# Optimization experiments

Hardware: AMD Instinct MI355X
Metric: run time of the kernel (lower is better)

Reference implementation:

```python
import jax, jax.numpy as jnp
from jax import lax
import numpy as np

S, ST, CI, K = 3, 2, 64, 7  # num_subset_S, num_subset_T, inter_channels, kernel_size


def _ln2(x, g, b, eps=1e-5):
    # LayerNorm over the last TWO dims (matches normalized_shape=[L, C])
    m = x.mean(axis=(-2, -1), keepdims=True)
    v = x.var(axis=(-2, -1), keepdims=True)
    return (x - m) / jnp.sqrt(v + eps) * g + b


def setup_inputs() -> dict:
    key = jax.random.key(0)
    ks = jax.random.split(key, 8)
    N, V, T, C = 32, 25, 64, 256
    g = lambda i, shape: jax.random.normal(ks[i], shape, jnp.float32) * 0.02
    return {
        "x": jax.random.normal(ks[0], (N, V, T, C), jnp.float32),
        "Wqk_s": g(1, (C, 2 * S * CI)), "bqk_s": jnp.zeros((2 * S * CI,), jnp.float32),
        "alphas": jnp.ones((1, 1, 1, S), jnp.float32),
        "attention0s": jnp.ones((1, V, V, S), jnp.float32) / V,
        "Wo_s": g(2, (S * C, C)), "bo_s": jnp.zeros((C,), jnp.float32),
        "g_os": jnp.ones((T, C), jnp.float32), "b_os": jnp.zeros((T, C), jnp.float32),
        "Wff_s": g(3, (C, C)), "bff_s": jnp.zeros((C,), jnp.float32),
        "g_ffs": jnp.ones((T, C), jnp.float32), "b_ffs": jnp.zeros((T, C), jnp.float32),
        "Wqk_t": g(4, (C, 4 * ST * CI)), "bqk_t": jnp.zeros((4 * ST * CI,), jnp.float32),
        "alphat_f": jnp.ones((1, 1, 1, ST), jnp.float32),
        "alphat_b": jnp.ones((1, 1, 1, ST), jnp.float32),
        "Wo_t": g(5, (2 * ST * C, C)), "bo_t": jnp.zeros((C,), jnp.float32),
        "g_ot": jnp.ones((V, C), jnp.float32), "b_ot": jnp.zeros((V, C), jnp.float32),
        "Wff_t": g(6, (C, C)), "bff_t": jnp.zeros((C,), jnp.float32),
        "g_fft": jnp.ones((V, C), jnp.float32), "b_fft": jnp.zeros((V, C), jnp.float32),
        "conv_w": g(7, (C, C, K, 1)), "conv_b": jnp.zeros((C,), jnp.float32),
        "bn_g": jnp.ones((C,), jnp.float32), "bn_b": jnp.zeros((C,), jnp.float32),
        "bn_m": jnp.zeros((C,), jnp.float32), "bn_v": jnp.ones((C,), jnp.float32),
    }


def reference(x, Wqk_s, bqk_s, alphas, attention0s, Wo_s, bo_s, g_os, b_os,
              Wff_s, bff_s, g_ffs, b_ffs, Wqk_t, bqk_t, alphat_f, alphat_b,
              Wo_t, bo_t, g_ot, b_ot, Wff_t, bff_t, g_fft, b_fft,
              conv_w, conv_b, bn_g, bn_b, bn_m, bn_v):
    N, V, T, C = x.shape
    gelu = lambda a: jax.nn.gelu(a, approximate=False)
    # ---- spatial multi-subset attention ----
    qk = (x @ Wqk_s + bqk_s).reshape(N, V, T, CI, 2 * S)
    q, k = qk[..., :S], qk[..., S:]
    att = jnp.tanh(jnp.einsum('nutcs,nvtcs->nuvs', q, k) / (CI * T)) * alphas + attention0s
    y = jnp.einsum('nutc,nuvs->nvtcs', x, att).reshape(N, V, T, S * C)
    y = gelu(x + _ln2(y @ Wo_s + bo_s, g_os, b_os))       # out_nets + residual (downs1=id)
    y = gelu(x + _ln2(y @ Wff_s + bff_s, g_ffs, b_ffs))   # ff_nets  + residual (downs2=id)
    y = y.transpose(0, 2, 1, 3)                            # (N,T,V,C)
    # ---- directed temporal attention ----
    qkt = (y @ Wqk_t + bqk_t).reshape(N, T, V, CI, 4 * ST)
    q_f, q_b = qkt[..., :ST], qkt[..., ST:2 * ST]
    k_f, k_b = qkt[..., 2 * ST:3 * ST], qkt[..., 3 * ST:]
    bmask = jnp.triu(jnp.ones((T, T), x.dtype))            # backward_mask; forward = transpose
    att_b = jnp.tanh(jnp.einsum('ntvcs,nqvcs->ntqs', q_b, k_b) / (CI * V)) * alphat_b * bmask[None, :, :, None]
    att_f = jnp.tanh(jnp.einsum('ntvcs,nqvcs->ntqs', q_f, k_f) / (CI * V)) * alphat_f * bmask.T[None, :, :, None]
    z_f = jnp.einsum('ntvc,ntqs->nqvcs', y, att_f).reshape(N, T, V, ST * C)
    z_b = jnp.einsum('ntvc,ntqs->nqvcs', y, att_b).reshape(N, T, V, ST * C)
    z = jnp.concatenate([z_f, z_b], axis=-1)               # (N,T,V,4C)
    z = gelu(y + _ln2(z @ Wo_t + bo_t, g_ot, b_ot))        # out_nett + residual (downt1=id)
    z = gelu(y + _ln2(z @ Wff_t + bff_t, g_fft, b_fft))    # ff_nett  + residual (downt2=id)
    # ---- TCN tail: (N,T,V,C) -> nctv ----
    zc = z.transpose(0, 3, 1, 2)                           # (N,C,T,V)
    pad = (K - 1) // 2
    z1 = lax.conv_general_dilated(zc, conv_w, (1, 1), [(pad, pad), (0, 0)],
                                  dimension_numbers=('NCHW', 'OIHW', 'NCHW'))
    z1 = z1 + conv_b[None, :, None, None]
    z1 = (z1 - bn_m[None, :, None, None]) / jnp.sqrt(bn_v + 1e-5)[None, :, None, None]
    z1 = z1 * bn_g[None, :, None, None] + bn_b[None, :, None, None]  # BatchNorm2d (eval)
    z1 = gelu(zc + z1)                                     # downt3 = identity
    return z1.transpose(0, 3, 2, 1)                        # nctv -> nvtc, (N,V,T,C)
```

## Files before the change

kernel.cpp:

```cpp
#include <hip/hip_runtime.h>

static constexpr int N_ = 32, V_ = 25, T_ = 64, C_ = 256;
static constexpr int S_ = 3, ST_ = 2, CI_ = 64, K_ = 7;
static constexpr int M_  = N_ * V_ * T_;
static constexpr int TC_ = T_ * C_;
static constexpr int VC_ = V_ * C_;
static constexpr long TOT_ = (long)M_ * C_;
static constexpr long PLANE_ = 2048L * 1600;

typedef __bf16 bf16x8 __attribute__((ext_vector_type(8)));
typedef float  f32x4  __attribute__((ext_vector_type(4)));

__device__ __forceinline__ float gelu_f(float x) {
    return 0.5f * x * (1.0f + erff(x * 0.70710678118654752f));
}
__device__ __forceinline__ ushort f2bf(float x) {
    uint u = __float_as_uint(x);
    u += 0x7fffu + ((u >> 16) & 1u);
    return (ushort)(u >> 16);
}
__device__ __forceinline__ float bf2f(ushort h) { return __uint_as_float((uint)h << 16); }

__device__ __forceinline__ int lofs(int row, int chunk) {
    return row * 32 + ((chunk ^ ((row >> 1) & 3)) << 3);
// ... 9 lines not shown
    hi[idx] = h;
    lo[idx] = f2bf(x - bf2f(h));
}
__global__ void prep_conv(const float* __restrict__ cw,
                          ushort* __restrict__ hi, ushort* __restrict__ lo) {
    int idx = blockIdx.x * 256 + threadIdx.x;
    if (idx >= K_ * C_ * C_) return;
    int kh = idx / (C_ * C_);
    int rem = idx % (C_ * C_);
    int o = rem >> 8, i = rem & 255;
    float x = cw[((long)o * C_ + i) * K_ + kh];
    ushort h = f2bf(x);
    hi[idx] = h;
    lo[idx] = f2bf(x - bf2f(h));
}

__global__ __launch_bounds__(256) void gemm_mfma(
    const float* __restrict__ A, int lda,
    const ushort* __restrict__ Wh, const ushort* __restrict__ Wl, int Kc,
    const float* __restrict__ bias,
    float* __restrict__ Out, int Nc)
{
    __shared__ ushort Ah[128 * 32], Al[128 * 32], Bh[128 * 32], Bl[128 * 32];
    const int tid = threadIdx.x;
    const int row0 = blockIdx.y * 128, col0 = blockIdx.x * 128;
    const int lane = tid & 63;
    const int wid = tid >> 6, wm = wid >> 1, wn = wid & 1;
    const int fr = lane & 15, fc = lane >> 4;
    const int r0 = tid >> 2, c0 = tid & 3;
    const int r1 = (tid + 256) >> 2, c1 = c0;
    const float*  arow0 = A + (long)(row0 + r0) * lda + c0 * 8;
    const float*  arow1 = A + (long)(row0 + r1) * lda + c1 * 8;
    const ushort* wrow0h = Wh + (long)(col0 + r0) * Kc + c0 * 8;
    const ushort* wrow0l = Wl + (long)(col0 + r0) * Kc + c0 * 8;
    const ushort* wrow1h = Wh + (long)(col0 + r1) * Kc + c1 * 8;
    const ushort* wrow1l = Wl + (long)(col0 + r1) * Kc + c1 * 8;
    const int la0 = lofs(r0, c0), la1 = lofs(r1, c1);

    float4 pa0, pa1, pa2, pa3;
    uint4 pw0h, pw0l, pw1h, pw1l;
    #define LOADK(k0) do { \
        pa0 = *(const float4*)(arow0 + (k0));      pa1 = *(const float4*)(arow0 + (k0) + 4); \
        pa2 = *(const float4*)(arow1 + (k0));      pa3 = *(const float4*)(arow1 + (k0) + 4); \
        pw0h = *(const uint4*)(wrow0h + (k0));     pw0l = *(const uint4*)(wrow0l + (k0)); \
        pw1h = *(const uint4*)(wrow1h + (k0));     pw1l = *(const uint4*)(wrow1l + (k0)); \
    } while (0)

    LOADK(0);
    f32x4 acc[4][4] = {};
    for (int k0 = 0; k0 < Kc; k0 += 32) {
        __syncthreads();
        {
            float f0[8] = {pa0.x, pa0.y, pa0.z, pa0.w, pa1.x, pa1.y, pa1.z, pa1.w};
            float f1[8] = {pa2.x, pa2.y, pa2.z, pa2.w, pa3.x, pa3.y, pa3.z, pa3.w};
            uint h0[4], l0[4], h1[4], l1[4];
            #pragma unroll
            for (int e = 0; e < 4; ++e) {
                ushort ha = f2bf(f0[2*e]), hb = f2bf(f0[2*e+1]);
                l0[e] = (uint)f2bf(f0[2*e] - bf2f(ha)) | ((uint)f2bf(f0[2*e+1] - bf2f(hb)) << 16);
                h0[e] = (uint)ha | ((uint)hb << 16);
                ushort hc = f2bf(f1[2*e]), hd = f2bf(f1[2*e+1]);
                l1[e] = (uint)f2bf(f1[2*e] - bf2f(hc)) | ((uint)f2bf(f1[2*e+1] - bf2f(hd)) << 16);
                h1[e] = (uint)hc | ((uint)hd << 16);
            }
            *(uint4*)&Ah[la0] = make_uint4(h0[0], h0[1], h0[2], h0[3]);
            *(uint4*)&Al[la0] = make_uint4(l0[0], l0[1], l0[2], l0[3]);
            *(uint4*)&Ah[la1] = make_uint4(h1[0], h1[1], h1[2], h1[3]);
            *(uint4*)&Al[la1] = make_uint4(l1[0], l1[1], l1[2], l1[3]);
            *(uint4*)&Bh[la0] = pw0h;  *(uint4*)&Bl[la0] = pw0l;
            *(uint4*)&Bh[la1] = pw1h;  *(uint4*)&Bl[la1] = pw1l;
        }
        __syncthreads();
        if (k0 + 32 < Kc) LOADK(k0 + 32);
        bf16x8 fah[4], fal[4];
        #pragma unroll
        for (int i = 0; i < 4; ++i) {
            int rA = wm * 64 + i * 16 + fr;
            int oA = lofs(rA, fc);
            fah[i] = *(bf16x8*)&Ah[oA];
            fal[i] = *(bf16x8*)&Al[oA];
        }
        #pragma unroll
        for (int j = 0; j < 4; ++j) {
            int rW = wn * 64 + j * 16 + fr;
            int oW = lofs(rW, fc);
            bf16x8 wh = *(bf16x8*)&Bh[oW];
            bf16x8 wl = *(bf16x8*)&Bl[oW];
            #pragma unroll
            for (int i = 0; i < 4; ++i) {
                acc[i][j] = __builtin_amdgcn_mfma_f32_16x16x32_bf16(fah[i], wh, acc[i][j], 0, 0, 0);
                acc[i][j] = __builtin_amdgcn_mfma_f32_16x16x32_bf16(fah[i], wl, acc[i][j], 0, 0, 0);
                acc[i][j] = __builtin_amdgcn_mfma_f32_16x16x32_bf16(fal[i], wh, acc[i][j], 0, 0, 0);
            }
        }
    }
    #undef LOADK
    float bv[4]; int colv[4];
    #pragma unroll
    for (int j = 0; j < 4; ++j) {
        colv[j] = col0 + wn * 64 + j * 16 + fr;
        bv[j] = bias ? bias[colv[j]] : 0.0f;
    }
    #pragma unroll
    for (int i = 0; i < 4; ++i) {
        long rbase = row0 + wm * 64 + i * 16 + fc * 4;
        #pragma unroll
        for (int r = 0; r < 4; ++r) {
            long ob = (rbase + r) * (long)Nc;
            #pragma unroll
            for (int j = 0; j < 4; ++j)
                Out[ob + colv[j]] = acc[i][j][r] + bv[j];
        }
    }
}

__global__ __launch_bounds__(256) void conv_bn_gelu(
    const float* __restrict__ Z,
    const ushort* __restrict__ Wh, const ushort* __restrict__ Wl,
    const float* __restrict__ conv_b, const float* __restrict__ bn_g,
    const float* __restrict__ bn_b,  const float* __restrict__ bn_m,
    const float* __restrict__ bn_v,
    float* __restrict__ Out)
{
    __shared__ ushort Ah[128 * 32], Al[128 * 32], Bh[128 * 32], Bl[128 * 32];
    const int tid = threadIdx.x;
    const int row0 = blockIdx.y * 128, col0 = blockIdx.x * 128;
    const int lane = tid & 63;
    const int wid = tid >> 6, wm = wid >> 1, wn = wid & 1;
    const int fr = lane & 15, fc = lane >> 4;
    const int r0 = tid >> 2, c0 = tid & 3;
    const int r1 = (tid + 256) >> 2, c1 = c0;
    const int la0 = lofs(r0, c0), la1 = lofs(r1, c1);
    const int m0 = row0 + r0, m1 = row0 + r1;
    const int t0g = (m0 / V_) % T_, t1g = (m1 / V_) % T_;

    float4 pa0, pa1, pa2, pa3;
    uint4 pw0h, pw0l, pw1h, pw1l;
    auto loadk = [&](int kt) {
        const int kh = kt >> 3, kc = (kt & 7) * 32, d = kh - 3;
        const float z4[4] = {0, 0, 0, 0};
        if (t0g + d >= 0 && t0g + d < T_) {
            const float* zr = Z + (long)(m0 + d * V_) * C_ + kc + c0 * 8;
            pa0 = *(const float4*)zr; pa1 = *(const float4*)(zr + 4);
        } else { pa0 = *(const float4*)z4; pa1 = *(const float4*)z4; }
        if (t1g + d >= 0 && t1g + d < T_) {
            const float* zr = Z + (long)(m1 + d * V_) * C_ + kc + c1 * 8;
            pa2 = *(const float4*)zr; pa3 = *(const float4*)(zr + 4);
        } else { pa2 = *(const float4*)z4; pa3 = *(const float4*)z4; }
        const ushort* w0 = Wh + (long)kh * C_ * C_ + (long)(col0 + r0) * C_ + kc + c0 * 8;
        const ushort* w1 = Wh + (long)kh * C_ * C_ + (long)(col0 + r1) * C_ + kc + c1 * 8;
        const ushort* v0 = Wl + (long)kh * C_ * C_ + (long)(col0 + r0) * C_ + kc + c0 * 8;
        const ushort* v1 = Wl + (long)kh * C_ * C_ + (long)(col0 + r1) * C_ + kc + c1 * 8;
        pw0h = *(const uint4*)w0; pw0l = *(const uint4*)v0;
        pw1h = *(const uint4*)w1; pw1l = *(const uint4*)v1;
    };

    loadk(0);
    f32x4 acc[4][4] = {};
    for (int kt = 0; kt < K_ * 8; ++kt) {
        __syncthreads();
        {
            float f0[8] = {pa0.x, pa0.y, pa0.z, pa0.w, pa1.x, pa1.y, pa1.z, pa1.w};
            float f1[8] = {pa2.x, pa2.y, pa2.z, pa2.w, pa3.x, pa3.y, pa3.z, pa3.w};
            uint h0[4], l0[4], h1[4], l1[4];
            #pragma unroll
            for (int e = 0; e < 4; ++e) {
                ushort ha = f2bf(f0[2*e]), hb = f2bf(f0[2*e+1]);
                l0[e] = (uint)f2bf(f0[2*e] - bf2f(ha)) | ((uint)f2bf(f0[2*e+1] - bf2f(hb)) << 16);
                h0[e] = (uint)ha | ((uint)hb << 16);
                ushort hc = f2bf(f1[2*e]), hd = f2bf(f1[2*e+1]);
                l1[e] = (uint)f2bf(f1[2*e] - bf2f(hc)) | ((uint)f2bf(f1[2*e+1] - bf2f(hd)) << 16);
                h1[e] = (uint)hc | ((uint)hd << 16);
            }
            *(uint4*)&Ah[la0] = make_uint4(h0[0], h0[1], h0[2], h0[3]);
            *(uint4*)&Al[la0] = make_uint4(l0[0], l0[1], l0[2], l0[3]);
            *(uint4*)&Ah[la1] = make_uint4(h1[0], h1[1], h1[2], h1[3]);
            *(uint4*)&Al[la1] = make_uint4(l1[0], l1[1], l1[2], l1[3]);
            *(uint4*)&Bh[la0] = pw0h;  *(uint4*)&Bl[la0] = pw0l;
            *(uint4*)&Bh[la1] = pw1h;  *(uint4*)&Bl[la1] = pw1l;
        }
        __syncthreads();
        if (kt + 1 < K_ * 8) loadk(kt + 1);
        bf16x8 fah[4], fal[4];
        #pragma unroll
        for (int i = 0; i < 4; ++i) {
            int rA = wm * 64 + i * 16 + fr;
            int oA = lofs(rA, fc);
            fah[i] = *(bf16x8*)&Ah[oA];
            fal[i] = *(bf16x8*)&Al[oA];
        }
        #pragma unroll
        for (int j = 0; j < 4; ++j) {
            int rW = wn * 64 + j * 16 + fr;
            int oW = lofs(rW, fc);
            bf16x8 wh = *(bf16x8*)&Bh[oW];
            bf16x8 wl = *(bf16x8*)&Bl[oW];
            #pragma unroll
            for (int i = 0; i < 4; ++i) {
                acc[i][j] = __builtin_amdgcn_mfma_f32_16x16x32_bf16(fah[i], wh, acc[i][j], 0, 0, 0);
                acc[i][j] = __builtin_amdgcn_mfma_f32_16x16x32_bf16(fah[i], wl, acc[i][j], 0, 0, 0);
                acc[i][j] = __builtin_amdgcn_mfma_f32_16x16x32_bf16(fal[i], wh, acc[i][j], 0, 0, 0);
            }
        }
    }
    float cbv[4], scv[4], shv[4]; int colv[4];
    #pragma unroll
    for (int j = 0; j < 4; ++j) {
        int c = col0 + wn * 64 + j * 16 + fr;
        colv[j] = c;
// ... 4 lines not shown
    }
    #pragma unroll
    for (int i = 0; i < 4; ++i)
        #pragma unroll
        for (int r = 0; r < 4; ++r) {
            int m = row0 + wm * 64 + i * 16 + fc * 4 + r;
            int n = m / (T_ * V_);
            int rem = m % (T_ * V_);
            int t = rem / V_, v = rem % V_;
            long ob = (((long)n * V_ + v) * T_ + t) * C_;
            long zb = (long)m * C_;
            #pragma unroll
            for (int j = 0; j < 4; ++j) {
                float cv = acc[i][j][r] + cbv[j];
                float bn = cv * scv[j] + shv[j];
                Out[ob + colv[j]] = gelu_f(Z[zb + colv[j]] + bn);
            }
        }
}

__global__ void zero_f32(float* __restrict__ p, int n) {
    int i = blockIdx.x * 256 + threadIdx.x;
    if (i < n) p[i] = 0.0f;
}

__global__ __launch_bounds__(256) void att_s_partial(
    const float* __restrict__ QK,
    float* __restrict__ attPre)
{
    const int n = blockIdx.x;
    const int tg = blockIdx.y;
// ... 50 lines not shown
        a[s][uv] = attS[((long)n * V_ * V_ + uv) * S_ + s];
    }
    __syncthreads();
    float acc[V_] = {};
    for (int u = 0; u < V_; ++u) {
        const float* g = G + ((long)((n * V_ + u) * T_) + t) * 768 + c;
        float v0 = g[0], v1 = g[256], v2 = g[512];
        const float* a0 = &a[0][u * V_], *a1 = &a[1][u * V_], *a2 = &a[2][u * V_];
        #pragma unroll
        for (int v = 0; v < V_; ++v)
            acc[v] += a0[v] * v0 + a1[v] * v1 + a2[v] * v2;
    }
    const float b = bias[c];
    for (int v = 0; v < V_; ++v)
        P[((long)(n * V_ + v) * T_ + t) * C_ + c] = acc[v] + b;
}

__global__ void qkt_repack(const float* __restrict__ QKT,
                           ushort* __restrict__ QPh, ushort* __restrict__ QPl) {
    long idx = (long)blockIdx.x * 256 + threadIdx.x;
    if (idx >= (long)M_ * CI_) return;
    int m = (int)(idx >> 6), ci = (int)(idx & 63);
    int n = m / (T_ * V_);
    int rem = m % (T_ * V_);
    int t = rem / V_, v = rem % V_;
    const float* src = QKT + (long)m * 512 + ci * 8;
    float4 s0 = *(const float4*)src;
    float4 s1 = *(const float4*)(src + 4);
    float f[8] = {s0.x, s0.y, s0.z, s0.w, s1.x, s1.y, s1.z, s1.w};
    long rowk = ((long)(n * T_ + t)) * 1600 + v * 64 + ci;
    #pragma unroll
    for (int chan = 0; chan < 8; ++chan) {
        ushort h = f2bf(f[chan]);
        QPh[(long)chan * PLANE_ + rowk] = h;
        QPl[(long)chan * PLANE_ + rowk] = f2bf(f[chan] - bf2f(h));
    }
}

__global__ __launch_bounds__(256) void att_t_mfma(
    const ushort* __restrict__ QPh, const ushort* __restrict__ QPl,
    float* __restrict__ part)
{
    const int ks = blockIdx.x, pair = blockIdx.y, n = blockIdx.z;
    const int kbeg = (ks * 50) / 4, kend = ((ks + 1) * 50) / 4;
    __shared__ ushort Qh[64 * 32], Ql[64 * 32], Kh[64 * 32], Kl[64 * 32];
    const int tid = threadIdx.x;
    const int lane = tid & 63;
    const int wid = tid >> 6, wm = wid >> 1, wn = wid & 1;
    const int fr = lane & 15, fc = lane >> 4;
    const int tr = tid >> 2, tc = tid & 3;
    const long rowoff = ((long)n * T_ + tr) * 1600 + tc * 8;
// ... 11 lines not shown
    f32x4 acc[2][2] = {};
    for (int kstep = kbeg; kstep < kend; ++kstep) {
        __syncthreads();
        *(uint4*)&Qh[la] = pqh;  *(uint4*)&Ql[la] = pql;
        *(uint4*)&Kh[la] = pkh;  *(uint4*)&Kl[la] = pkl;
        __syncthreads();
        if (kstep + 1 < kend) {
            pqh = *(const uint4*)(qh_g + (kstep + 1) * 32);
            pql = *(const uint4*)(ql_g + (kstep + 1) * 32);
            pkh = *(const uint4*)(kh_g + (kstep + 1) * 32);
            pkl = *(const uint4*)(kl_g + (kstep + 1) * 32);
        }
        bf16x8 ah[2], al[2];
        #pragma unroll
        for (int i = 0; i < 2; ++i) {
            int rA = wm * 32 + i * 16 + fr;
            int oA = lofs(rA, fc);
            ah[i] = *(bf16x8*)&Qh[oA];
            al[i] = *(bf16x8*)&Ql[oA];
        }
        #pragma unroll
        for (int j = 0; j < 2; ++j) {
            int rB = wn * 32 + j * 16 + fr;
            int oB = lofs(rB, fc);
            bf16x8 bh = *(bf16x8*)&Kh[oB];
            bf16x8 bl = *(bf16x8*)&Kl[oB];
            #pragma unroll
            for (int i = 0; i < 2; ++i) {
                acc[i][j] = __builtin_amdgcn_mfma_f32_16x16x32_bf16(ah[i], bh, acc[i][j], 0, 0, 0);
                acc[i][j] = __builtin_amdgcn_mfma_f32_16x16x32_bf16(ah[i], bl, acc[i][j], 0, 0, 0);
                acc[i][j] = __builtin_amdgcn_mfma_f32_16x16x32_bf16(al[i], bh, acc[i][j], 0, 0, 0);
            }
        }
    }
    float* pb = part + (((long)ks * N_ + n) * 4 + pair) * 4096;
    #pragma unroll
    for (int i = 0; i < 2; ++i)
        #pragma unroll
        for (int r = 0; r < 4; ++r) {
// ... 50 lines not shown
        const float* g = G + ((long)((n * T_ + t) * V_) + v) * 512 + c;
        float v0 = g[0], v1 = g[256];
        const float* ar0 = &a[t * T_ + ty * 16];
        const float* ar1 = ar0 + T_ * T_;
        #pragma unroll
        for (int i = 0; i < 16; ++i) acc[i] += ar0[i] * v0 + ar1[i] * v1;
    }
    for (int i = 0; i < 16; ++i) {
        int q = ty * 16 + i;
        long idx = ((long)n * T_ + q) * VC_ + col;
        if (INIT) P[idx] = acc[i] + bias[c];
        else      P[idx] += acc[i];
    }
}

template <bool TR>
__global__ __launch_bounds__(256) void ln_res_gelu_TC(
    const float* __restrict__ P, const float* __restrict__ X,
    const float* __restrict__ G, const float* __restrict__ B,
    float* __restrict__ Out)
{
    const int g = blockIdx.x;
    const int n = g / V_, v = g % V_;
    const float* p = P + (long)g * TC_;
    const float* x = X + (long)g * TC_;
    float s = 0.f, ss = 0.f;
    for (int i = threadIdx.x; i < TC_; i += 256) { float a = p[i]; s += a; ss += a * a; }
    __shared__ float rs[4], rss[4];
    #pragma unroll
    for (int off = 32; off > 0; off >>= 1) { s += __shfl_down(s, off); ss += __shfl_down(ss, off); }
    if ((threadIdx.x & 63) == 0) { rs[threadIdx.x >> 6] = s; rss[threadIdx.x >> 6] = ss; }
    __syncthreads();
    s = rs[0] + rs[1] + rs[2] + rs[3];
    ss = rss[0] + rss[1] + rss[2] + rss[3];
    const float mean = s * (1.0f / TC_);
    const float var  = ss * (1.0f / TC_) - mean * mean;
    const float rstd = rsqrtf(var + 1e-5f);
    for (int i = threadIdx.x; i < TC_; i += 256) {
        float val = (p[i] - mean) * rstd * G[i] + B[i];
        float r = gelu_f(x[i] + val);
        if (TR) {
            int t = i >> 8, c = i & 255;
            Out[(((long)n * T_ + t) * V_ + v) * C_ + c] = r;
        } else {
            Out[(long)g * TC_ + i] = r;
        }
    }
}

__global__ __launch_bounds__(256) void ln_res_gelu_VC(
    const float* __restrict__ P, const float* __restrict__ X,
    const float* __restrict__ G, const float* __restrict__ B,
    float* __restrict__ Out)
{
    const int g = blockIdx.x;
    const float* p = P + (long)g * VC_;
    const float* x = X + (long)g * VC_;
    float s = 0.f, ss = 0.f;
    for (int i = threadIdx.x; i < VC_; i += 256) { float a = p[i]; s += a; ss += a * a; }
    __shared__ float rs[4], rss[4];
    #pragma unroll
    for (int off = 32; off > 0; off >>= 1) { s += __shfl_down(s, off); ss += __shfl_down(ss, off); }
    if ((threadIdx.x & 63) == 0) { rs[threadIdx.x >> 6] = s; rss[threadIdx.x >> 6] = ss; }
    __syncthreads();
    s = rs[0] + rs[1] + rs[2] + rs[3];
    ss = rss[0] + rss[1] + rss[2] + rss[3];
    const float mean = s * (1.0f / VC_);
    const float var  = ss * (1.0f / VC_) - mean * mean;
    const float rstd = rsqrtf(var + 1e-5f);
    for (int i = threadIdx.x; i < VC_; i += 256) {
        float val = (p[i] - mean) * rstd * G[i] + B[i];
        Out[(long)g * VC_ + i] = gelu_f(x[i] + val);
    }
}

extern "C" void kernel_launch(void* const* d_in, const int* in_sizes, int n_in,
                              void* d_out, int out_size, void* d_ws, size_t ws_size,
                              hipStream_t stream)
{
    const float* x        = (const float*)d_in[0];
    const float* Wqk_s    = (const float*)d_in[1];
    const float* bqk_s    = (const float*)d_in[2];
    const float* alphas   = (const float*)d_in[3];
    const float* att0s    = (const float*)d_in[4];
    const float* Wo_s     = (const float*)d_in[5];
    const float* bo_s     = (const float*)d_in[6];
    const float* g_os     = (const float*)d_in[7];
// ... 9 lines not shown
    const float* Wo_t     = (const float*)d_in[17];
    const float* bo_t     = (const float*)d_in[18];
    const float* g_ot     = (const float*)d_in[19];
    const float* b_ot     = (const float*)d_in[20];
    const float* Wff_t    = (const float*)d_in[21];
    const float* bff_t    = (const float*)d_in[22];
    const float* g_fft    = (const float*)d_in[23];
    const float* b_fft    = (const float*)d_in[24];
    const float* conv_w   = (const float*)d_in[25];
    const float* conv_b   = (const float*)d_in[26];
    const float* bn_g     = (const float*)d_in[27];
    const float* bn_b     = (const float*)d_in[28];
    const float* bn_m     = (const float*)d_in[29];
    const float* bn_v     = (const float*)d_in[30];

    float* B  = (float*)d_ws;
    float* B0  = B;
    float* B13 = B + TOT_;
    float* B26 = B + 2 * TOT_;
    float* B39 = B + 3 * TOT_;
    float* RA  = B + 4 * TOT_;
    float* attPre = RA;
    float* attS   = attPre + N_*V_*V_*S_;
    float* attF   = attS   + N_*V_*V_*S_;
    float* attB   = attF   + (long)N_*2*T_*T_;
    float* part   = attB   + (long)N_*2*T_*T_;
    ushort* wp = (ushort*)(part + 4L*N_*4*4096);
    ushort* qs_h = wp;  wp += 384*256;   ushort* qs_l = wp;  wp += 384*256;
    ushort* os_h = wp;  wp += 768*256;   ushort* os_l = wp;  wp += 768*256;
    ushort* fs_h = wp;  wp += 256*256;   ushort* fs_l = wp;  wp += 256*256;
    ushort* qt_h = wp;  wp += 512*256;   ushort* qt_l = wp;  wp += 512*256;
    ushort* ot0_h= wp;  wp += 512*256;   ushort* ot0_l= wp;  wp += 512*256;
    ushort* ot1_h= wp;  wp += 512*256;   ushort* ot1_l= wp;  wp += 512*256;
    ushort* ft_h = wp;  wp += 256*256;   ushort* ft_l = wp;  wp += 256*256;
    ushort* cv_h = wp;  wp += K_*256*256; ushort* cv_l = wp;
    ushort* QPh = (ushort*)B26;
    ushort* QPl = QPh + 8 * PLANE_;
    float* YT = (float*)d_out;

    auto prepw = [&](const float* W, int Kc, int Nc, ushort* h, ushort* l) {
        prep_w<<<(Kc*Nc + 255)/256, 256, 0, stream>>>(W, Kc, Nc, h, l);
    };
    prepw(Wqk_s, C_, 384, qs_h, qs_l);
    prepw(Wo_s,  C_, 768, os_h, os_l);
    prepw(Wff_s, C_, 256, fs_h, fs_l);
    prepw(Wqk_t, C_, 512, qt_h, qt_l);
    prepw(Wo_t,                      C_, 512, ot0_h, ot0_l);
    prepw(Wo_t + (long)ST_*C_*C_,    C_, 512, ot1_h, ot1_l);
    prepw(Wff_t, C_, 256, ft_h, ft_l);
    prep_conv<<<(K_*C_*C_ + 255)/256, 256, 0, stream>>>(conv_w, cv_h, cv_l);

    gemm_mfma<<<dim3(384/128, M_/128), 256, 0, stream>>>(x, C_, qs_h, qs_l, C_, bqk_s, B0, 384);
    zero_f32<<<(N_*V_*V_*S_ + 255)/256, 256, 0, stream>>>(attPre, N_*V_*V_*S_);
    att_s_partial<<<dim3(N_, 8), 256, 0, stream>>>(B0, attPre);
    att_s_final<<<(N_*V_*V_*S_ + 255)/256, 256, 0, stream>>>(attPre, alphas, att0s, attS);
    gemm_mfma<<<dim3(768/128, M_/128), 256, 0, stream>>>(x, C_, os_h, os_l, C_, nullptr, B0, 768);
    vmix_all<<<dim3(T_, N_), 256, 0, stream>>>(B0, attS, bo_s, B39);
    ln_res_gelu_TC<false><<<N_*V_, 256, 0, stream>>>(B39, x, g_os, b_os, B0);
    gemm_mfma<<<dim3(256/128, M_/128), 256, 0, stream>>>(B0, C_, fs_h, fs_l, C_, bff_s, B13, 256);
    ln_res_gelu_TC<true><<<N_*V_, 256, 0, stream>>>(B13, x, g_ffs, b_ffs, YT);

    gemm_mfma<<<dim3(512/128, M_/128), 256, 0, stream>>>(YT, C_, qt_h, qt_l, C_, bqk_t, B0, 512);
    qkt_repack<<<(int)(((long)M_*CI_ + 255)/256), 256, 0, stream>>>(B0, QPh, QPl);
    att_t_mfma<<<dim3(4, 4, N_), 256, 0, stream>>>(QPh, QPl, part);
    att_t_final<<<(N_*4*4096 + 255)/256, 256, 0, stream>>>(part, alphat_f, alphat_b, attF, attB);
    gemm_mfma<<<dim3(512/128, M_/128), 256, 0, stream>>>(YT, C_, ot0_h, ot0_l, C_, nullptr, B26, 512);
    tmix_all<true><<<dim3(VC_/64, N_), 256, 0, stream>>>(B26, attF, bo_t, B0);
    gemm_mfma<<<dim3(512/128, M_/128), 256, 0, stream>>>(YT, C_, ot1_h, ot1_l, C_, nullptr, B26, 512);
    tmix_all<false><<<dim3(VC_/64, N_), 256, 0, stream>>>(B26, attB, nullptr, B0);
    ln_res_gelu_VC<<<N_*T_, 256, 0, stream>>>(B0, YT, g_ot, b_ot, B13);
    gemm_mfma<<<dim3(256/128, M_/128), 256, 0, stream>>>(B13, C_, ft_h, ft_l, C_, bff_t, B26, 256);
    ln_res_gelu_VC<<<N_*T_, 256, 0, stream>>>(B26, YT, g_fft, b_fft, B39);

    conv_bn_gelu<<<dim3(C_/128, M_/128), 256, 0, stream>>>(B39, cv_h, cv_l, conv_b, bn_g, bn_b, bn_m, bn_v, (float*)d_out);
}
```

Before: 1.480 ms.

## Pre-split activations into bf16 hi/lo planes in producer kernels, feeding GEMMs directly

```diff
diff --git a/kernel.cpp b/kernel.cpp
--- a/kernel.cpp
+++ b/kernel.cpp
@@ -7,6 +7,7 @@
 static constexpr int VC_ = V_ * C_;
 static constexpr long TOT_ = (long)M_ * C_;
 static constexpr long PLANE_ = 2048L * 1600;
+static constexpr int TP_ = T_ + 6;
 
 typedef __bf16 bf16x8 __attribute__((ext_vector_type(8)));
 typedef float  f32x4  __attribute__((ext_vector_type(4)));
@@ -47,12 +48,33 @@
     hi[idx] = h;
     lo[idx] = f2bf(x - bf2f(h));
 }
-
-__global__ __launch_bounds__(256) void gemm_mfma(
-    const float* __restrict__ A, int lda,
-    const ushort* __restrict__ Wh, const ushort* __restrict__ Wl, int Kc,
+__global__ void prep_x(const float* __restrict__ X,
+                       ushort* __restrict__ Xh, ushort* __restrict__ Xl) {
+    long i = (long)blockIdx.x * 256 + threadIdx.x;
+    if (i >= TOT_) return;
+    float v = X[i];
+    ushort h = f2bf(v);
+    Xh[i] = h;
+    Xl[i] = f2bf(v - bf2f(h));
+}
+__global__ void zero_pad(ushort* __restrict__ Zph, ushort* __restrict__ Zpl) {
+    int idx = blockIdx.x * 256 + threadIdx.x;
+    if (idx >= N_ * 6 * V_ * C_) return;
+    int n = idx / (6 * V_ * C_);
+    int rem = idx % (6 * V_ * C_);
+    int tpi = rem / (V_ * C_), vc = rem % (V_ * C_);
+    int tp = (tpi < 3) ? tpi : (64 + tpi);
+    long o = ((long)(n * TP_ + tp) * V_) * C_ + vc;
+    Zph[o] = 0; Zpl[o] = 0;
+}
+
+template <bool PLANES>
+__global__ __launch_bounds__(256) void gemm_bf(
+    const ushort* __restrict__ Agh, const ushort* __restrict__ Agl,
+    const ushort* __restrict__ Wh,  const ushort* __restrict__ Wl,
     const float* __restrict__ bias,
-    float* __restrict__ Out, int Nc)
+    float* __restrict__ Out, int Nc,
+    ushort* __restrict__ Ph, ushort* __restrict__ Pl)
 {
     __shared__ ushort Ah[128 * 32], Al[128 * 32], Bh[128 * 32], Bl[128 * 32];
     const int tid = threadIdx.x;
@@ -61,62 +83,39 @@
     const int wid = tid >> 6, wm = wid >> 1, wn = wid & 1;
     const int fr = lane & 15, fc = lane >> 4;
     const int r0 = tid >> 2, c0 = tid & 3;
-    const int r1 = (tid + 256) >> 2, c1 = c0;
-    const float*  arow0 = A + (long)(row0 + r0) * lda + c0 * 8;
-    const float*  arow1 = A + (long)(row0 + r1) * lda + c1 * 8;
-    const ushort* wrow0h = Wh + (long)(col0 + r0) * Kc + c0 * 8;
-    const ushort* wrow0l = Wl + (long)(col0 + r0) * Kc + c0 * 8;
-    const ushort* wrow1h = Wh + (long)(col0 + r1) * Kc + c1 * 8;
-    const ushort* wrow1l = Wl + (long)(col0 + r1) * Kc + c1 * 8;
-    const int la0 = lofs(r0, c0), la1 = lofs(r1, c1);
-
-    float4 pa0, pa1, pa2, pa3;
-    uint4 pw0h, pw0l, pw1h, pw1l;
-    #define LOADK(k0) do { \
-        pa0 = *(const float4*)(arow0 + (k0));      pa1 = *(const float4*)(arow0 + (k0) + 4); \
-        pa2 = *(const float4*)(arow1 + (k0));      pa3 = *(const float4*)(arow1 + (k0) + 4); \
-        pw0h = *(const uint4*)(wrow0h + (k0));     pw0l = *(const uint4*)(wrow0l + (k0)); \
-        pw1h = *(const uint4*)(wrow1h + (k0));     pw1l = *(const uint4*)(wrow1l + (k0)); \
-    } while (0)
-
-    LOADK(0);
+    const long a0off = (long)(row0 + r0) * 256 + c0 * 8;
+    const long a1off = (long)(row0 + r0 + 64) * 256 + c0 * 8;
+    const long w0off = (long)(col0 + r0) * 256 + c0 * 8;
+    const long w1off = (long)(col0 + r0 + 64) * 256 + c0 * 8;
+    const int la0 = lofs(r0, c0), la1 = lofs(r0 + 64, c0);
+
+    uint4 p0, p1, p2, p3, p4, p5, p6, p7;
+    #define LD(k0) do { \
+        p0 = *(const uint4*)(Agh + a0off + (k0)); p1 = *(const uint4*)(Agh + a1off + (k0)); \
+        p2 = *(const uint4*)(Agl + a0off + (k0)); p3 = *(const uint4*)(Agl + a1off + (k0)); \
+        p4 = *(const uint4*)(Wh  + w0off + (k0)); p5 = *(const uint4*)(Wh  + w1off + (k0)); \
+        p6 = *(const uint4*)(Wl  + w0off + (k0)); p7 = *(const uint4*)(Wl  + w1off + (k0)); } while (0)
+
+    LD(0);
     f32x4 acc[4][4] = {};
-    for (int k0 = 0; k0 < Kc; k0 += 32) {
-        __syncthreads();
-        {
-            float f0[8] = {pa0.x, pa0.y, pa0.z, pa0.w, pa1.x, pa1.y, pa1.z, pa1.w};
-            float f1[8] = {pa2.x, pa2.y, pa2.z, pa2.w, pa3.x, pa3.y, pa3.z, pa3.w};
-            uint h0[4], l0[4], h1[4], l1[4];
-            #pragma unroll
-            for (int e = 0; e < 4; ++e) {
-                ushort ha = f2bf(f0[2*e]), hb = f2bf(f0[2*e+1]);
-                l0[e] = (uint)f2bf(f0[2*e] - bf2f(ha)) | ((uint)f2bf(f0[2*e+1] - bf2f(hb)) << 16);
-                h0[e] = (uint)ha | ((uint)hb << 16);
-                ushort hc = f2bf(f1[2*e]), hd = f2bf(f1[2*e+1]);
-                l1[e] = (uint)f2bf(f1[2*e] - bf2f(hc)) | ((uint)f2bf(f1[2*e+1] - bf2f(hd)) << 16);
-                h1[e] = (uint)hc | ((uint)hd << 16);
-            }
-            *(uint4*)&Ah[la0] = make_uint4(h0[0], h0[1], h0[2], h0[3]);
-            *(uint4*)&Al[la0] = make_uint4(l0[0], l0[1], l0[2], l0[3]);
-            *(uint4*)&Ah[la1] = make_uint4(h1[0], h1[1], h1[2], h1[3]);
-            *(uint4*)&Al[la1] = make_uint4(l1[0], l1[1], l1[2], l1[3]);
-            *(uint4*)&Bh[la0] = pw0h;  *(uint4*)&Bl[la0] = pw0l;
-            *(uint4*)&Bh[la1] = pw1h;  *(uint4*)&Bl[la1] = pw1l;
-        }
-        __syncthreads();
-        if (k0 + 32 < Kc) LOADK(k0 + 32);
+    for (int k0 = 0; k0 < 256; k0 += 32) {
+        __syncthreads();
+        *(uint4*)&Ah[la0] = p0;  *(uint4*)&Ah[la1] = p1;
+        *(uint4*)&Al[la0] = p2;  *(uint4*)&Al[la1] = p3;
+        *(uint4*)&Bh[la0] = p4;  *(uint4*)&Bh[la1] = p5;
+        *(uint4*)&Bl[la0] = p6;  *(uint4*)&Bl[la1] = p7;
+        __syncthreads();
+        if (k0 + 32 < 256) LD(k0 + 32);
         bf16x8 fah[4], fal[4];
         #pragma unroll
         for (int i = 0; i < 4; ++i) {
-            int rA = wm * 64 + i * 16 + fr;
-            int oA = lofs(rA, fc);
+            int oA = lofs(wm * 64 + i * 16 + fr, fc);
             fah[i] = *(bf16x8*)&Ah[oA];
             fal[i] = *(bf16x8*)&Al[oA];
         }
         #pragma unroll
         for (int j = 0; j < 4; ++j) {
-            int rW = wn * 64 + j * 16 + fr;
-            int oW = lofs(rW, fc);
+            int oW = lofs(wn * 64 + j * 16 + fr, fc);
             bf16x8 wh = *(bf16x8*)&Bh[oW];
             bf16x8 wl = *(bf16x8*)&Bl[oW];
             #pragma unroll
@@ -127,28 +126,52 @@
             }
         }
     }
-    #undef LOADK
+    #undef LD
     float bv[4]; int colv[4];
     #pragma unroll
     for (int j = 0; j < 4; ++j) {
         colv[j] = col0 + wn * 64 + j * 16 + fr;
         bv[j] = bias ? bias[colv[j]] : 0.0f;
     }
-    #pragma unroll
-    for (int i = 0; i < 4; ++i) {
-        long rbase = row0 + wm * 64 + i * 16 + fc * 4;
-        #pragma unroll
-        for (int r = 0; r < 4; ++r) {
-            long ob = (rbase + r) * (long)Nc;
+    if (!PLANES) {
+        #pragma unroll
+        for (int i = 0; i < 4; ++i) {
+            long rbase = row0 + wm * 64 + i * 16 + fc * 4;
             #pragma unroll
-            for (int j = 0; j < 4; ++j)
-                Out[ob + colv[j]] = acc[i][j][r] + bv[j];
+            for (int r = 0; r < 4; ++r) {
+                long ob = (rbase + r) * (long)Nc;
+                #pragma unroll
+                for (int j = 0; j < 4; ++j)
+                    Out[ob + colv[j]] = acc[i][j][r] + bv[j];
+            }
+        }
+    } else {
+        #pragma unroll
+        for (int i = 0; i < 4; ++i) {
+            #pragma unroll
+            for (int r = 0; r < 4; ++r) {
+                int m = row0 + wm * 64 + i * 16 + fc * 4 + r;
+                int n = m / (T_ * V_);
+                int rem = m % (T_ * V_);
+                int t = rem / V_, v = rem % V_;
+                long rk = ((long)(n * T_ + t)) * 1600 + v * 64;
+                #pragma unroll
+                for (int j = 0; j < 4; ++j) {
+                    int col = colv[j];
+                    int chan = col & 7, ci = col >> 3;
+                    float val = acc[i][j][r] + bv[j];
+                    ushort h = f2bf(val);
+                    Ph[(long)chan * PLANE_ + rk + ci] = h;
+                    Pl[(long)chan * PLANE_ + rk + ci] = f2bf(val - bf2f(h));
+                }
+            }
         }
     }
 }
 
 __global__ __launch_bounds__(256) void conv_bn_gelu(
-    const float* __restrict__ Z,
+    const ushort* __restrict__ Zph, const ushort* __restrict__ Zpl,
+    const float* __restrict__ Zres,
     const ushort* __restrict__ Wh, const ushort* __restrict__ Wl,
     const float* __restrict__ conv_b, const float* __restrict__ bn_g,
     const float* __restrict__ bn_b,  const float* __restrict__ bn_m,
@@ -162,70 +185,51 @@
     const int wid = tid >> 6, wm = wid >> 1, wn = wid & 1;
     const int fr = lane & 15, fc = lane >> 4;
     const int r0 = tid >> 2, c0 = tid & 3;
-    const int r1 = (tid + 256) >> 2, c1 = c0;
-    const int la0 = lofs(r0, c0), la1 = lofs(r1, c1);
-    const int m0 = row0 + r0, m1 = row0 + r1;
-    const int t0g = (m0 / V_) % T_, t1g = (m1 / V_) % T_;
-
-    float4 pa0, pa1, pa2, pa3;
-    uint4 pw0h, pw0l, pw1h, pw1l;
+    const int la0 = lofs(r0, c0), la1 = lofs(r0 + 64, c0);
+    const int m0 = row0 + r0, m1 = row0 + r0 + 64;
+    const int n0 = m0 / (T_ * V_), q0 = m0 % (T_ * V_);
+    const int n1 = m1 / (T_ * V_), q1 = m1 % (T_ * V_);
+    const long a0base = ((long)(n0 * TP_ + q0 / V_) * V_ + q0 % V_) * 256 + c0 * 8;
+    const long a1base = ((long)(n1 * TP_ + q1 / V_) * V_ + q1 % V_) * 256 + c0 * 8;
+    const long w0base = (long)(col0 + r0) * 256 + c0 * 8;
+    const long w1base = (long)(col0 + r0 + 64) * 256 + c0 * 8;
+
+    uint4 p0, p1, p2, p3, p4, p5, p6, p7;
     auto loadk = [&](int kt) {
-        const int kh = kt >> 3, kc = (kt & 7) * 32, d = kh - 3;
-        const float z4[4] = {0, 0, 0, 0};
-        if (t0g + d >= 0 && t0g + d < T_) {
-            const float* zr = Z + (long)(m0 + d * V_) * C_ + kc + c0 * 8;
-            pa0 = *(const float4*)zr; pa1 = *(const float4*)(zr + 4);
-        } else { pa0 = *(const float4*)z4; pa1 = *(const float4*)z4; }
-        if (t1g + d >= 0 && t1g + d < T_) {
-            const float* zr = Z + (long)(m1 + d * V_) * C_ + kc + c1 * 8;
-            pa2 = *(const float4*)zr; pa3 = *(const float4*)(zr + 4);
-        } else { pa2 = *(const float4*)z4; pa3 = *(const float4*)z4; }
-        const ushort* w0 = Wh + (long)kh * C_ * C_ + (long)(col0 + r0) * C_ + kc + c0 * 8;
-        const ushort* w1 = Wh + (long)kh * C_ * C_ + (long)(col0 + r1) * C_ + kc + c1 * 8;
-        const ushort* v0 = Wl + (long)kh * C_ * C_ + (long)(col0 + r0) * C_ + kc + c0 * 8;
-        const ushort* v1 = Wl + (long)kh * C_ * C_ + (long)(col0 + r1) * C_ + kc + c1 * 8;
-        pw0h = *(const uint4*)w0; pw0l = *(const uint4*)v0;
-        pw1h = *(const uint4*)w1; pw1l = *(const uint4*)v1;
+        const int kh = kt >> 3;
+        const long kc = (kt & 7) * 32;
+        const long ao = (long)kh * V_ * 256;
+        p0 = *(const uint4*)(Zph + a0base + ao + kc);
+        p1 = *(const uint4*)(Zph + a1base + ao + kc);
+        p2 = *(const uint4*)(Zpl + a0base + ao + kc);
+        p3 = *(const uint4*)(Zpl + a1base + ao + kc);
+        const long wo = (long)kh * 65536 + kc;
+        p4 = *(const uint4*)(Wh + w0base + wo);
+        p5 = *(const uint4*)(Wh + w1base + wo);
+        p6 = *(const uint4*)(Wl + w0base + wo);
+        p7 = *(const uint4*)(Wl + w1base + wo);
     };
 
     loadk(0);
     f32x4 acc[4][4] = {};
     for (int kt = 0; kt < K_ * 8; ++kt) {
         __syncthreads();
-        {
-            float f0[8] = {pa0.x, pa0.y, pa0.z, pa0.w, pa1.x, pa1.y, pa1.z, pa1.w};
-            float f1[8] = {pa2.x, pa2.y, pa2.z, pa2.w, pa3.x, pa3.y, pa3.z, pa3.w};
-            uint h0[4], l0[4], h1[4], l1[4];
-            #pragma unroll
-            for (int e = 0; e < 4; ++e) {
-                ushort ha = f2bf(f0[2*e]), hb = f2bf(f0[2*e+1]);
-                l0[e] = (uint)f2bf(f0[2*e] - bf2f(ha)) | ((uint)f2bf(f0[2*e+1] - bf2f(hb)) << 16);
-                h0[e] = (uint)ha | ((uint)hb << 16);
-                ushort hc = f2bf(f1[2*e]), hd = f2bf(f1[2*e+1]);
-                l1[e] = (uint)f2bf(f1[2*e] - bf2f(hc)) | ((uint)f2bf(f1[2*e+1] - bf2f(hd)) << 16);
-                h1[e] = (uint)hc | ((uint)hd << 16);
-            }
-            *(uint4*)&Ah[la0] = make_uint4(h0[0], h0[1], h0[2], h0[3]);
-            *(uint4*)&Al[la0] = make_uint4(l0[0], l0[1], l0[2], l0[3]);
-            *(uint4*)&Ah[la1] = make_uint4(h1[0], h1[1], h1[2], h1[3]);
-            *(uint4*)&Al[la1] = make_uint4(l1[0], l1[1], l1[2], l1[3]);
-            *(uint4*)&Bh[la0] = pw0h;  *(uint4*)&Bl[la0] = pw0l;
-            *(uint4*)&Bh[la1] = pw1h;  *(uint4*)&Bl[la1] = pw1l;
-        }
+        *(uint4*)&Ah[la0] = p0;  *(uint4*)&Ah[la1] = p1;
+        *(uint4*)&Al[la0] = p2;  *(uint4*)&Al[la1] = p3;
+        *(uint4*)&Bh[la0] = p4;  *(uint4*)&Bh[la1] = p5;
+        *(uint4*)&Bl[la0] = p6;  *(uint4*)&Bl[la1] = p7;
         __syncthreads();
         if (kt + 1 < K_ * 8) loadk(kt + 1);
         bf16x8 fah[4], fal[4];
         #pragma unroll
         for (int i = 0; i < 4; ++i) {
-            int rA = wm * 64 + i * 16 + fr;
-            int oA = lofs(rA, fc);
+            int oA = lofs(wm * 64 + i * 16 + fr, fc);
             fah[i] = *(bf16x8*)&Ah[oA];
             fal[i] = *(bf16x8*)&Al[oA];
         }
         #pragma unroll
         for (int j = 0; j < 4; ++j) {
-            int rW = wn * 64 + j * 16 + fr;
-            int oW = lofs(rW, fc);
+            int oW = lofs(wn * 64 + j * 16 + fr, fc);
             bf16x8 wh = *(bf16x8*)&Bh[oW];
             bf16x8 wl = *(bf16x8*)&Bl[oW];
             #pragma unroll
@@ -260,7 +264,7 @@
             for (int j = 0; j < 4; ++j) {
                 float cv = acc[i][j][r] + cbv[j];
                 float bn = cv * scv[j] + shv[j];
-                Out[ob + colv[j]] = gelu_f(Z[zb + colv[j]] + bn);
+                Out[ob + colv[j]] = gelu_f(Zres[zb + colv[j]] + bn);
             }
         }
 }
@@ -341,27 +345,6 @@
     const float b = bias[c];
     for (int v = 0; v < V_; ++v)
         P[((long)(n * V_ + v) * T_ + t) * C_ + c] = acc[v] + b;
-}
-
-__global__ void qkt_repack(const float* __restrict__ QKT,
-                           ushort* __restrict__ QPh, ushort* __restrict__ QPl) {
-    long idx = (long)blockIdx.x * 256 + threadIdx.x;
-    if (idx >= (long)M_ * CI_) return;
-    int m = (int)(idx >> 6), ci = (int)(idx & 63);
-    int n = m / (T_ * V_);
-    int rem = m % (T_ * V_);
-    int t = rem / V_, v = rem % V_;
-    const float* src = QKT + (long)m * 512 + ci * 8;
-    float4 s0 = *(const float4*)src;
-    float4 s1 = *(const float4*)(src + 4);
-    float f[8] = {s0.x, s0.y, s0.z, s0.w, s1.x, s1.y, s1.z, s1.w};
-    long rowk = ((long)(n * T_ + t)) * 1600 + v * 64 + ci;
-    #pragma unroll
-    for (int chan = 0; chan < 8; ++chan) {
-        ushort h = f2bf(f[chan]);
-        QPh[(long)chan * PLANE_ + rowk] = h;
-        QPl[(long)chan * PLANE_ + rowk] = f2bf(f[chan] - bf2f(h));
-    }
 }
 
 __global__ __launch_bounds__(256) void att_t_mfma(
@@ -403,15 +386,13 @@
         bf16x8 ah[2], al[2];
         #pragma unroll
         for (int i = 0; i < 2; ++i) {
-            int rA = wm * 32 + i * 16 + fr;
-            int oA = lofs(rA, fc);
+            int oA = lofs(wm * 32 + i * 16 + fr, fc);
             ah[i] = *(bf16x8*)&Qh[oA];
             al[i] = *(bf16x8*)&Ql[oA];
         }
         #pragma unroll
         for (int j = 0; j < 2; ++j) {
-            int rB = wn * 32 + j * 16 + fr;
-            int oB = lofs(rB, fc);
+            int oB = lofs(wn * 32 + j * 16 + fr, fc);
             bf16x8 bh = *(bf16x8*)&Kh[oB];
             bf16x8 bl = *(bf16x8*)&Kl[oB];
             #pragma unroll
@@ -492,63 +473,96 @@
     }
 }
 
-template <bool TR>
-__global__ __launch_bounds__(256) void ln_res_gelu_TC(
+#define LN_STATS(PBASE, L)                                                     \
+    float s = 0.f, ss = 0.f;                                                   \
+    for (int i = threadIdx.x; i < L; i += 256) { float a = (PBASE)[i]; s += a; ss += a * a; } \
+    __shared__ float rs[4], rss[4];                                            \
+    _Pragma("unroll")                                                          \
+    for (int off = 32; off > 0; off >>= 1) { s += __shfl_down(s, off); ss += __shfl_down(ss, off); } \
+    if ((threadIdx.x & 63) == 0) { rs[threadIdx.x >> 6] = s; rss[threadIdx.x >> 6] = ss; } \
+    __syncthreads();                                                           \
+    s = rs[0] + rs[1] + rs[2] + rs[3];                                         \
+    ss = rss[0] + rss[1] + rss[2] + rss[3];                                    \
+    const float mean = s * (1.0f / (L));                                       \
+    const float var  = ss * (1.0f / (L)) - mean * mean;                        \
+    const float rstd = rsqrtf(var + 1e-5f);
+
+__global__ __launch_bounds__(256) void ln_tc_y(
     const float* __restrict__ P, const float* __restrict__ X,
     const float* __restrict__ G, const float* __restrict__ B,
-    float* __restrict__ Out)
+    ushort* __restrict__ Oh, ushort* __restrict__ Ol)
+{
+    const int g = blockIdx.x;
+    const float* p = P + (long)g * TC_;
+    const float* x = X + (long)g * TC_;
+    LN_STATS(p, TC_)
+    for (int i = threadIdx.x; i < TC_; i += 256) {
+        float val = (p[i] - mean) * rstd * G[i] + B[i];
+        float r = gelu_f(x[i] + val);
+        ushort h = f2bf(r);
+        Oh[(long)g * TC_ + i] = h;
+        Ol[(long)g * TC_ + i] = f2bf(r - bf2f(h));
+    }
+}
+
+__global__ __launch_bounds__(256) void ln_tc_yt(
+    const float* __restrict__ P, const float* __restrict__ X,
+    const float* __restrict__ G, const float* __restrict__ B,
+    float* __restrict__ OutF, ushort* __restrict__ Oh, ushort* __restrict__ Ol)
 {
     const int g = blockIdx.x;
     const int n = g / V_, v = g % V_;
     const float* p = P + (long)g * TC_;
     const float* x = X + (long)g * TC_;
-    float s = 0.f, ss = 0.f;
-    for (int i = threadIdx.x; i < TC_; i += 256) { float a = p[i]; s += a; ss += a * a; }
-    __shared__ float rs[4], rss[4];
-    #pragma unroll
-    for (int off = 32; off > 0; off >>= 1) { s += __shfl_down(s, off); ss += __shfl_down(ss, off); }
-    if ((threadIdx.x & 63) == 0) { rs[threadIdx.x >> 6] = s; rss[threadIdx.x >> 6] = ss; }
-    __syncthreads();
-    s = rs[0] + rs[1] + rs[2] + rs[3];
-    ss = rss[0] + rss[1] + rss[2] + rss[3];
-    const float mean = s * (1.0f / TC_);
-    const float var  = ss * (1.0f / TC_) - mean * mean;
-    const float rstd = rsqrtf(var + 1e-5f);
+    LN_STATS(p, TC_)
     for (int i = threadIdx.x; i < TC_; i += 256) {
         float val = (p[i] - mean) * rstd * G[i] + B[i];
         float r = gelu_f(x[i] + val);
-        if (TR) {
-            int t = i >> 8, c = i & 255;
-            Out[(((long)n * T_ + t) * V_ + v) * C_ + c] = r;
-        } else {
-            Out[(long)g * TC_ + i] = r;
-        }
-    }
-}
-
-__global__ __launch_bounds__(256) void ln_res_gelu_VC(
+        int t = i >> 8, c = i & 255;
+        long o = (((long)n * T_ + t) * V_ + v) * C_ + c;
+        OutF[o] = r;
+        ushort h = f2bf(r);
+        Oh[o] = h;
+        Ol[o] = f2bf(r - bf2f(h));
+    }
+}
+
+__global__ __launch_bounds__(256) void ln_vc_z(
     const float* __restrict__ P, const float* __restrict__ X,
     const float* __restrict__ G, const float* __restrict__ B,
-    float* __restrict__ Out)
+    ushort* __restrict__ Oh, ushort* __restrict__ Ol)
 {
     const int g = blockIdx.x;
     const float* p = P + (long)g * VC_;
     const float* x = X + (long)g * VC_;
-    float s = 0.f, ss = 0.f;
-    for (int i = threadIdx.x; i < VC_; i += 256) { float a = p[i]; s += a; ss += a * a; }
-    __shared__ float rs[4], rss[4];
-    #pragma unroll
-    for (int off = 32; off > 0; off >>= 1) { s += __shfl_down(s, off); ss += __shfl_down(ss, off); }
-    if ((threadIdx.x & 63) == 0) { rs[threadIdx.x >> 6] = s; rss[threadIdx.x >> 6] = ss; }
-    __syncthreads();
-    s = rs[0] + rs[1] + rs[2] + rs[3];
-    ss = rss[0] + rss[1] + rss[2] + rss[3];
-    const float mean = s * (1.0f / VC_);
-    const float var  = ss * (1.0f / VC_) - mean * mean;
-    const float rstd = rsqrtf(var + 1e-5f);
+    LN_STATS(p, VC_)
     for (int i = threadIdx.x; i < VC_; i += 256) {
         float val = (p[i] - mean) * rstd * G[i] + B[i];
-        Out[(long)g * VC_ + i] = gelu_f(x[i] + val);
+        float r = gelu_f(x[i] + val);
+        ushort h = f2bf(r);
+        Oh[(long)g * VC_ + i] = h;
+        Ol[(long)g * VC_ + i] = f2bf(r - bf2f(h));
+    }
+}
+
+__global__ __launch_bounds__(256) void ln_vc_z2(
+    const float* __restrict__ P, const float* __restrict__ X,
+    const float* __restrict__ G, const float* __restrict__ B,
+    float* __restrict__ OutF, ushort* __restrict__ Zph, ushort* __restrict__ Zpl)
+{
+    const int g = blockIdx.x;
+    const int n = g / T_, t = g % T_;
+    const float* p = P + (long)g * VC_;
+    const float* x = X + (long)g * VC_;
+    LN_STATS(p, VC_)
+    const long pbase = ((long)(n * TP_ + t + 3) * V_) * C_;
+    for (int i = threadIdx.x; i < VC_; i += 256) {
+        float val = (p[i] - mean) * rstd * G[i] + B[i];
+        float r = gelu_f(x[i] + val);
+        OutF[(long)g * VC_ + i] = r;
+        ushort h = f2bf(r);
+        Zph[pbase + i] = h;
+        Zpl[pbase + i] = f2bf(r - bf2f(h));
     }
 }
 
@@ -588,13 +602,13 @@
     const float* bn_m     = (const float*)d_in[29];
     const float* bn_v     = (const float*)d_in[30];
 
-    float* B  = (float*)d_ws;
-    float* B0  = B;
-    float* B13 = B + TOT_;
-    float* B26 = B + 2 * TOT_;
-    float* B39 = B + 3 * TOT_;
-    float* RA  = B + 4 * TOT_;
-    float* attPre = RA;
+    float* Bp  = (float*)d_ws;
+    float* R0f = Bp;
+    float* R1f = Bp + TOT_;
+    float* R2f = Bp + 2 * TOT_;
+    float* R3f = Bp + 3 * TOT_;
+    float* SM  = Bp + 4 * TOT_;
+    float* attPre = SM;
     float* attS   = attPre + N_*V_*V_*S_;
     float* attF   = attS   + N_*V_*V_*S_;
     float* attB   = attF   + (long)N_*2*T_*T_;
@@ -608,43 +622,50 @@
     ushort* ot1_h= wp;  wp += 512*256;   ushort* ot1_l= wp;  wp += 512*256;
     ushort* ft_h = wp;  wp += 256*256;   ushort* ft_l = wp;  wp += 256*256;
     ushort* cv_h = wp;  wp += K_*256*256; ushort* cv_l = wp;
-    ushort* QPh = (ushort*)B26;
-    ushort* QPl = QPh + 8 * PLANE_;
+
+    ushort* xh  = (ushort*)R3f;  ushort* xl  = xh  + TOT_;
+    ushort* Yh  = (ushort*)R0f;  ushort* Yl  = Yh  + TOT_;
+    ushort* YTh = (ushort*)R0f;  ushort* YTl = YTh + TOT_;
+    ushort* QPh = (ushort*)R1f;  ushort* QPl = (ushort*)R2f;
+    ushort* Zh  = (ushort*)R1f;  ushort* Zl  = Zh  + TOT_;
+    ushort* Zph = (ushort*)R0f;
+    ushort* Zpl = Zph + (long)N_ * TP_ * V_ * C_;
     float* YT = (float*)d_out;
 
-    auto prepw = [&](const float* W, int Kc, int Nc, ushort* h, ushort* l) {
-        prep_w<<<(Kc*Nc + 255)/256, 256, 0, stream>>>(W, Kc, Nc, h, l);
+    auto prepw = [&](const float* W, int Nc, ushort* h, ushort* l) {
+        prep_w<<<(256*Nc + 255)/256, 256, 0, stream>>>(W, 256, Nc, h, l);
     };
-    prepw(Wqk_s, C_, 384, qs_h, qs_l);
-    prepw(Wo_s,  C_, 768, os_h, os_l);
-    prepw(Wff_s, C_, 256, fs_h, fs_l);
-    prepw(Wqk_t, C_, 512, qt_h, qt_l);
-    prepw(Wo_t,                      C_, 512, ot0_h, ot0_l);
-    prepw(Wo_t + (long)ST_*C_*C_,    C_, 512, ot1_h, ot1_l);
-    prepw(Wff_t, C_, 256, ft_h, ft_l);
+    prepw(Wqk_s, 384, qs_h, qs_l);
+    prepw(Wo_s,  768, os_h, os_l);
+    prepw(Wff_s, 256, fs_h, fs_l);
+    prepw(Wqk_t, 512, qt_h, qt_l);
+    prepw(Wo_t,                   512, ot0_h, ot0_l);
+    prepw(Wo_t + (long)ST_*C_*C_, 512, ot1_h, ot1_l);
+    prepw(Wff_t, 256, ft_h, ft_l);
     prep_conv<<<(K_*C_*C_ + 255)/256, 256, 0, stream>>>(conv_w, cv_h, cv_l);
-
-    gemm_mfma<<<dim3(384/128, M_/128), 256, 0, stream>>>(x, C_, qs_h, qs_l, C_, bqk_s, B0, 384);
+    prep_x<<<(int)((TOT_ + 255)/256), 256, 0, stream>>>(x, xh, xl);
+
+    gemm_bf<false><<<dim3(3, 400), 256, 0, stream>>>(xh, xl, qs_h, qs_l, bqk_s, R0f, 384, nullptr, nullptr);
     zero_f32<<<(N_*V_*V_*S_ + 255)/256, 256, 0, stream>>>(attPre, N_*V_*V_*S_);
-    att_s_partial<<<dim3(N_, 8), 256, 0, stream>>>(B0, attPre);
+    att_s_partial<<<dim3(N_, 8), 256, 0, stream>>>(R0f, attPre);
     att_s_final<<<(N_*V_*V_*S_ + 255)/256, 256, 0, stream>>>(attPre, alphas, att0s, attS);
-    gemm_mfma<<<dim3(768/128, M_/128), 256, 0, stream>>>(x, C_, os_h, os_l, C_, nullptr, B0, 768);
-    vmix_all<<<dim3(T_, N_), 256, 0, stream>>>(B0, attS, bo_s, B39);
-    ln_res_gelu_TC<false><<<N_*V_, 256, 0, stream>>>(B39, x, g_os, b_os, B0);
-    gemm_mfma<<<dim3(256/128, M_/128), 256, 0, stream>>>(B0, C_, fs_h, fs_l, C_, bff_s, B13, 256);
-    ln_res_gelu_TC<true><<<N_*V_, 256, 0, stream>>>(B13, x, g_ffs, b_ffs, YT);
-
-    gemm_mfma<<<dim3(512/128, M_/128), 256, 0, stream>>>(YT, C_, qt_h, qt_l, C_, bqk_t, B0, 512);
-    qkt_repack<<<(int)(((long)M_*CI_ + 255)/256), 256, 0, stream>>>(B0, QPh, QPl);
+    gemm_bf<false><<<dim3(6, 400), 256, 0, stream>>>(xh, xl, os_h, os_l, nullptr, R0f, 768, nullptr, nullptr);
+    vmix_all<<<dim3(T_, N_), 256, 0, stream>>>(R0f, attS, bo_s, R3f);
+    ln_tc_y<<<N_*V_, 256, 0, stream>>>(R3f, x, g_os, b_os, Yh, Yl);
+    gemm_bf<false><<<dim3(2, 400), 256, 0, stream>>>(Yh, Yl, fs_h, fs_l, bff_s, R1f, 256, nullptr, nullptr);
+    ln_tc_yt<<<N_*V_, 256, 0, stream>>>(R1f, x, g_ffs, b_ffs, YT, YTh, YTl);
+
+    gemm_bf<true><<<dim3(4, 400), 256, 0, stream>>>(YTh, YTl, qt_h, qt_l, bqk_t, nullptr, 512, QPh, QPl);
     att_t_mfma<<<dim3(4, 4, N_), 256, 0, stream>>>(QPh, QPl, part);
     att_t_final<<<(N_*4*4096 + 255)/256, 256, 0, stream>>>(part, alphat_f, alphat_b, attF, attB);
-    gemm_mfma<<<dim3(512/128, M_/128), 256, 0, stream>>>(YT, C_, ot0_h, ot0_l, C_, nullptr, B26, 512);
-    tmix_all<true><<<dim3(VC_/64, N_), 256, 0, stream>>>(B26, attF, bo_t, B0);
-    gemm_mfma<<<dim3(512/128, M_/128), 256, 0, stream>>>(YT, C_, ot1_h, ot1_l, C_, nullptr, B26, 512);
-    tmix_all<false><<<dim3(VC_/64, N_), 256, 0, stream>>>(B26, attB, nullptr, B0);
-    ln_res_gelu_VC<<<N_*T_, 256, 0, stream>>>(B0, YT, g_ot, b_ot, B13);
-    gemm_mfma<<<dim3(256/128, M_/128), 256, 0, stream>>>(B13, C_, ft_h, ft_l, C_, bff_t, B26, 256);
-    ln_res_gelu_VC<<<N_*T_, 256, 0, stream>>>(B26, YT, g_fft, b_fft, B39);
-
-    conv_bn_gelu<<<dim3(C_/128, M_/128), 256, 0, stream>>>(B39, cv_h, cv_l, conv_b, bn_g, bn_b, bn_m, bn_v, (float*)d_out);
-}
+    gemm_bf<false><<<dim3(4, 400), 256, 0, stream>>>(YTh, YTl, ot0_h, ot0_l, nullptr, R1f, 512, nullptr, nullptr);
+    tmix_all<true><<<dim3(VC_/64, N_), 256, 0, stream>>>(R1f, attF, bo_t, R3f);
+    gemm_bf<false><<<dim3(4, 400), 256, 0, stream>>>(YTh, YTl, ot1_h, ot1_l, nullptr, R1f, 512, nullptr, nullptr);
+    tmix_all<false><<<dim3(VC_/64, N_), 256, 0, stream>>>(R1f, attB, nullptr, R3f);
+    ln_vc_z<<<N_*T_, 256, 0, stream>>>(R3f, YT, g_ot, b_ot, Zh, Zl);
+    gemm_bf<false><<<dim3(2, 400), 256, 0, stream>>>(Zh, Zl, ft_h, ft_l, bff_t, R2f, 256, nullptr, nullptr);
+    zero_pad<<<(N_*6*V_*C_ + 255)/256, 256, 0, stream>>>(Zph, Zpl);
+    ln_vc_z2<<<N_*T_, 256, 0, stream>>>(R2f, YT, g_fft, b_fft, R3f, Zph, Zpl);
+
+    conv_bn_gelu<<<dim3(2, 400), 256, 0, stream>>>(Zph, Zpl, R3f, cv_h, cv_l, conv_b, bn_g, bn_b, bn_m, bn_v, (float*)d_out);
+}
```

Result: slower. 1.549 ms (+4.6%).
